# Optimization experiments

Hardware: AMD Instinct MI355X
Metric: run time of the kernel (lower is better)

## Reference

```python
import jax, jax.numpy as jnp
import numpy as np

B, SQ, SKV, D, H = 2, 2048, 2048, 1024, 16
DH = D // H


def setup_inputs() -> dict:
    key = jax.random.key(0)
    ks = jax.random.split(key, 4)
    s = 0.02
    return {
        "query_input": jax.random.normal(ks[0], (B, SQ, D), jnp.float32),
        "kv_input": jax.random.normal(ks[1], (B, SKV, D), jnp.float32),
        "Wq": jax.random.normal(ks[2], (D, D), jnp.float32) * s,
        "bq": jnp.zeros((D,), jnp.float32),
        "Wkv": jax.random.normal(ks[3], (D, 2 * D), jnp.float32) * s,
        "bkv": jnp.zeros((2 * D,), jnp.float32),
        "Wo": jax.random.normal(jax.random.fold_in(key, 7), (D, D), jnp.float32) * s,
        "bo": jnp.zeros((D,), jnp.float32),
    }


def reference(query_input, kv_input, Wq, bq, Wkv, bkv, Wo, bo):
    scale = 1.0 / jnp.sqrt(jnp.float32(DH))
    # Projections
    q = query_input @ Wq + bq                      # [B, SQ, D]
    kv = kv_input @ Wkv + bkv                      # [B, SKV, 2D]
    k, v = jnp.split(kv, 2, axis=-1)               # [B, SKV, D] each
    # Split heads: [B, H, S, DH]
    q = q.reshape(B, SQ, H, DH).transpose(0, 2, 1, 3)
    k = k.reshape(B, SKV, H, DH).transpose(0, 2, 1, 3)
    v = v.reshape(B, SKV, H, DH).transpose(0, 2, 1, 3)
    # Scores S = QK^T / sqrt(d_k)
    scores = jnp.einsum("bhqd,bhkd->bhqk", q, k) * scale
    attn = jax.nn.softmax(scores, axis=-1)
    out = jnp.einsum("bhqk,bhkd->bhqd", attn, v)   # [B, H, SQ, DH]
    out = out.transpose(0, 2, 1, 3).reshape(B, SQ, D)
    return out @ Wo + bo
```

## Files before the change

### kernel.cpp

```cpp
#include <hip/hip_runtime.h>

typedef unsigned short u16;
typedef unsigned int u32;
typedef __bf16 bf16x8 __attribute__((ext_vector_type(8)));
typedef float f32x4 __attribute__((ext_vector_type(4)));

#define QSCALE 0.18033688011112f

__device__ __forceinline__ u16 f2bf(float f) {
  u32 u = __builtin_bit_cast(u32, f);
  u += 0x7fffu + ((u >> 16) & 1u);
  return (u16)(u >> 16);
}

__device__ __forceinline__ bf16x8 as_bf16x8(uint4 v) {
  return __builtin_bit_cast(bf16x8, v);
}

__device__ __forceinline__ void async16(const void* g, void* l) {
  __builtin_amdgcn_global_load_lds(
      (__attribute__((address_space(1))) void*)(g),
      (__attribute__((address_space(3))) void*)(l), 16, 0, 0);
}

__global__ void prep_kernel(const float* __restrict__ xq, const float* __restrict__ xkv,
                            const float* __restrict__ Wq, const float* __restrict__ Wkv,
                            const float* __restrict__ Wo,
                            u16* __restrict__ Xq16, u16* __restrict__ Xkv16,
                            u16* __restrict__ WqT, u16* __restrict__ WkvT,
                            u16* __restrict__ WoT) {
  const int bid = blockIdx.x, tid = threadIdx.x;
  if (bid < 8192) {
    int i = bid * 256 + tid;
    const float* s; u16* d; int j;
    if (i < 1048576) { s = xq; d = Xq16; j = i; }
    else             { s = xkv; d = Xkv16; j = i - 1048576; }
    float4 v = ((const float4*)s)[j];
    ushort4 o;
    o.x = f2bf(v.x); o.y = f2bf(v.y); o.z = f2bf(v.z); o.w = f2bf(v.w);
    ((ushort4*)d)[j] = o;
    return;
  }
  const int b2 = bid - 8192;
  const int z = b2 >> 11, rem = b2 & 2047;
  const int by = rem >> 6, bx = rem & 63;
  const float* src; u16* dst; int Nd;
  if (z == 0)      { src = Wq;  dst = WqT;  Nd = 1024; }
  else if (z == 1) { src = Wkv; dst = WkvT; Nd = 2048; }
  else             { src = Wo;  dst = WoT;  Nd = 1024; }
  const int n0 = bx * 32, k0 = by * 32;
  if (n0 >= Nd) return;
  __shared__ float tile[32][33];
  const int tx = tid & 31, ty = tid >> 5;
#pragma unroll
  for (int j = 0; j < 4; ++j)
    tile[ty + 8 * j][tx] = src[(size_t)(k0 + ty + 8 * j) * Nd + n0 + tx];
  __syncthreads();
#pragma unroll
  for (int j = 0; j < 4; ++j)
    dst[(size_t)(n0 + ty + 8 * j) * 1024 + k0 + tx] = f2bf(tile[tx][ty + 8 * j]);
}

template <int MI>
static __device__ __forceinline__ void gemm_core(
    const u16* __restrict__ A, const u16* __restrict__ Bt, int m0,
    uint4* sA, uint4* sB, f32x4 (*acc)[4]) {
  const int tid = threadIdx.x;
  const int wv = tid >> 6, lane = tid & 63;
  const int quad = lane >> 4, l16 = lane & 15;
  const int wm = (wv >> 1) * (MI * 16), wn = (wv & 1) * 64;

  const int ib0 = wv * 128 + lane, ib1 = ib0 + 64;
  const int br0 = ib0 >> 2, bc0 = (ib0 & 3) ^ ((br0 >> 1) & 3);
  const int br1 = ib1 >> 2, bc1 = (ib1 & 3) ^ ((br1 >> 1) & 3);
  const u16* gB0 = Bt + (size_t)br0 * 1024 + bc0 * 8;
  const u16* gB1 = Bt + (size_t)br1 * 1024 + bc1 * 8;

  const int ia0 = wv * (MI * 32) + lane;
  const int ar0 = ia0 >> 2, ac0 = (ia0 & 3) ^ ((ar0 >> 1) & 3);
  const u16* gA0 = A + (size_t)(m0 + ar0) * 1024 + ac0 * 8;
  const int ia1 = ia0 + 64;
  const int ar1 = ia1 >> 2, ac1 = (ia1 & 3) ^ ((ar1 >> 1) & 3);
  const u16* gA1 = A + (size_t)(m0 + ar1) * 1024 + ac1 * 8;
  uint4* sAw = sA + wv * (MI * 32);
  uint4* sBw = sB + wv * 128;

  for (int k0 = 0; k0 < 1024; k0 += 32) {
    __syncthreads();
    async16(gA0 + k0, sAw);
    if (MI == 4) async16(gA1 + k0, sAw + 64);
    async16(gB0 + k0, sBw);
    async16(gB1 + k0, sBw + 64);
    __syncthreads();

    bf16x8 af[MI], bfr[4];
#pragma unroll
    for (int mi = 0; mi < MI; ++mi) {
      int r = wm + mi * 16 + l16;
      af[mi] = as_bf16x8(sA[r * 4 + (quad ^ ((r >> 1) & 3))]);
    }
#pragma unroll
    for (int ni = 0; ni < 4; ++ni) {
      int r = wn + ni * 16 + l16;
      bfr[ni] = as_bf16x8(sB[r * 4 + (quad ^ ((r >> 1) & 3))]);
    }
#pragma unroll
    for (int mi = 0; mi < MI; ++mi)
#pragma unroll
      for (int ni = 0; ni < 4; ++ni)
        acc[mi][ni] = __builtin_amdgcn_mfma_f32_16x16x32_bf16(
            af[mi], bfr[ni], acc[mi][ni], 0, 0, 0);
  }
}

__global__ __launch_bounds__(256, 2) void gemm_qkv(
    const u16* __restrict__ Xq, const u16* __restrict__ Xkv,
    const u16* __restrict__ WqT, const u16* __restrict__ WkvT,
    const float* __restrict__ bq, const float* __restrict__ bkv,
    u16* __restrict__ Qd, u16* __restrict__ Kd, u16* __restrict__ Vd) {
  __shared__ uint4 sA[512], sB[512];
  f32x4 acc[4][4] = {};
  const int n0 = blockIdx.x * 128, m0 = blockIdx.y * 128;
  const u16* A = (n0 < 1024) ? Xq : Xkv;
  const u16* Bt = (n0 < 1024) ? (WqT + (size_t)n0 * 1024)
                              : (WkvT + (size_t)(n0 - 1024) * 1024);
  const float* bias = (n0 < 1024) ? (bq + n0) : (bkv + (n0 - 1024));
  gemm_core<4>(A, Bt, m0, sA, sB, acc);

  const int tid = threadIdx.x, wv = tid >> 6, lane = tid & 63;
  const int quad = lane >> 4, l16 = lane & 15;
  const int wm = (wv >> 1) * 64, wn = (wv & 1) * 64;
  const int bb = m0 >> 11;
  const int gmb = m0 + wm + quad * 4;
  const int ssb = (m0 & 2047) + wm + quad * 4;
#pragma unroll
  for (int ni = 0; ni < 4; ++ni) {
    const int gn = n0 + wn + ni * 16 + l16;
    const float bvn = bias[wn + ni * 16 + l16];
    if (gn < 1024) {
      u16* base = Qd + gn;
#pragma unroll
      for (int mi = 0; mi < 4; ++mi)
#pragma unroll
        for (int r = 0; r < 4; ++r)
          base[(size_t)(gmb + mi * 16 + r) * 1024] = f2bf((acc[mi][ni][r] + bvn) * QSCALE);
    } else if (gn < 2048) {
      u16* base = Kd + (gn - 1024);
#pragma unroll
      for (int mi = 0; mi < 4; ++mi)
#pragma unroll
        for (int r = 0; r < 4; ++r)
          base[(size_t)(gmb + mi * 16 + r) * 1024] = f2bf(acc[mi][ni][r] + bvn);
    } else {
      const int col = gn - 2048, hh = col >> 6, dh = col & 63;
      u16* base = Vd + ((size_t)(bb * 16 + hh) * 64 + dh) * 2048 + ssb;
#pragma unroll
      for (int mi = 0; mi < 4; ++mi) {
        ushort4 o;
        o.x = f2bf(acc[mi][ni][0] + bvn);
        o.y = f2bf(acc[mi][ni][1] + bvn);
        o.z = f2bf(acc[mi][ni][2] + bvn);
        o.w = f2bf(acc[mi][ni][3] + bvn);
        *(ushort4*)(base + mi * 16) = o;
      }
    }
  }
}

__global__ __launch_bounds__(128, 3) void flash_attn(
    const u16* __restrict__ Q, const u16* __restrict__ K,
    const u16* __restrict__ V, u16* __restrict__ O) {
  __shared__ uint4 sK[512];
  __shared__ uint4 sV[512];
  __shared__ __align__(16) u16 sP[2][32][72];

  const int tid = threadIdx.x;
  const int wv = tid >> 6, lane = tid & 63;
  const int quad = lane >> 4, l16 = lane & 15;
  const int q0 = blockIdx.x * 64;
  const int h = blockIdx.y;

  const u16* Qb = Q + ((size_t)(blockIdx.z * 2048 + q0)) * 1024 + h * 64;
  const u16* Kb = K + ((size_t)(blockIdx.z * 2048)) * 1024 + h * 64;
  const u16* Vb = V + ((size_t)(blockIdx.z * 16 + h)) * 64 * 2048;

  bf16x8 qf[2][2];
#pragma unroll
  for (int rb = 0; rb < 2; ++rb) {
    const uint4* qp = (const uint4*)(Qb + (size_t)(wv * 32 + rb * 16 + l16) * 1024);
    qf[rb][0] = as_bf16x8(qp[quad]);
    qf[rb][1] = as_bf16x8(qp[4 + quad]);
  }

  f32x4 oacc[2][4] = {};
  f32x4 lsum[2] = {};
  const uint4 ones4 = {0x3F803F80u, 0x3F803F80u, 0x3F803F80u, 0x3F803F80u};
  const bf16x8 ones = as_bf16x8(ones4);

  const u16* gK[4]; const u16* gV[4];
#pragma unroll
  for (int j = 0; j < 4; ++j) {
    int i = wv * 256 + j * 64 + lane;
    int r = i >> 3;
    int ck = (i & 7) ^ ((r >> 2) & 7);
    int cv = (i & 7) ^ (r & 7);
    gK[j] = Kb + (size_t)r * 1024 + ck * 8;
    gV[j] = Vb + (size_t)r * 2048 + cv * 8;
  }
  uint4* sKw = sK + wv * 256;
  uint4* sVw = sV + wv * 256;

  for (int t = 0; t < 32; ++t) {
    const int skv0 = t * 64;
    __syncthreads();
#pragma unroll
    for (int j = 0; j < 4; ++j) {
      async16(gK[j] + (size_t)skv0 * 1024, sKw + j * 64);
      async16(gV[j] + skv0, sVw + j * 64);
    }
    __syncthreads();

    bf16x8 bK0[4], bK1[4];
#pragma unroll
    for (int ni = 0; ni < 4; ++ni) {
      int rr = l16 * 4 + ni;
      bK0[ni] = as_bf16x8(sK[rr * 8 + (quad ^ (l16 & 7))]);
      bK1[ni] = as_bf16x8(sK[rr * 8 + ((4 + quad) ^ (l16 & 7))]);
    }

#pragma unroll
    for (int rb = 0; rb < 2; ++rb) {
      f32x4 s4[4];
#pragma unroll
      for (int ni = 0; ni < 4; ++ni) {
        f32x4 a = {0.f, 0.f, 0.f, 0.f};
        a = __builtin_amdgcn_mfma_f32_16x16x32_bf16(qf[rb][0], bK0[ni], a, 0, 0, 0);
        a = __builtin_amdgcn_mfma_f32_16x16x32_bf16(qf[rb][1], bK1[ni], a, 0, 0, 0);
        s4[ni] = a;
      }
#pragma unroll
      for (int r = 0; r < 4; ++r) {
        u32 u0 = __builtin_bit_cast(u32, exp2f(s4[0][r])) + 0x8000u;
        u32 u1 = __builtin_bit_cast(u32, exp2f(s4[1][r])) + 0x8000u;
        u32 u2 = __builtin_bit_cast(u32, exp2f(s4[2][r])) + 0x8000u;
        u32 u3 = __builtin_bit_cast(u32, exp2f(s4[3][r])) + 0x8000u;
        uint2 pk;
        pk.x = (u0 >> 16) | (u1 & 0xFFFF0000u);
        pk.y = (u2 >> 16) | (u3 & 0xFFFF0000u);
        *(uint2*)&sP[wv][rb * 16 + quad * 4 + r][l16 * 4] = pk;
      }
    }

    bf16x8 vf0[4], vf1[4];
#pragma unroll
    for (int ni = 0; ni < 4; ++ni) {
      int rr = ni * 16 + l16;
      vf0[ni] = as_bf16x8(sV[rr * 8 + (quad ^ (rr & 7))]);
      vf1[ni] = as_bf16x8(sV[rr * 8 + ((4 + quad) ^ (rr & 7))]);
    }
#pragma unroll
    for (int rb = 0; rb < 2; ++rb) {
      bf16x8 pf0 = as_bf16x8(*(const uint4*)&sP[wv][rb * 16 + l16][quad * 8]);
      bf16x8 pf1 = as_bf16x8(*(const uint4*)&sP[wv][rb * 16 + l16][32 + quad * 8]);
      lsum[rb] = __builtin_amdgcn_mfma_f32_16x16x32_bf16(pf0, ones, lsum[rb], 0, 0, 0);
      lsum[rb] = __builtin_amdgcn_mfma_f32_16x16x32_bf16(pf1, ones, lsum[rb], 0, 0, 0);
#pragma unroll
      for (int ni = 0; ni < 4; ++ni) {
        oacc[rb][ni] = __builtin_amdgcn_mfma_f32_16x16x32_bf16(pf0, vf0[ni], oacc[rb][ni], 0, 0, 0);
        oacc[rb][ni] = __builtin_amdgcn_mfma_f32_16x16x32_bf16(pf1, vf1[ni], oacc[rb][ni], 0, 0, 0);
      }
    }
  }

#pragma unroll
  for (int rb = 0; rb < 2; ++rb) {
    u16* Ob = O + ((size_t)(blockIdx.z * 2048 + q0 + wv * 32 + rb * 16 + quad * 4)) * 1024
                + h * 64;
#pragma unroll
    for (int r = 0; r < 4; ++r) {
      float rl = 1.0f / lsum[rb][r];
#pragma unroll
      for (int ni = 0; ni < 4; ++ni)
        Ob[(size_t)r * 1024 + ni * 16 + l16] = f2bf(oacc[rb][ni][r] * rl);
    }
  }
}

__global__ __launch_bounds__(256, 2) void gemm_out(
    const u16* __restrict__ A, const u16* __restrict__ Bt,
    const float* __restrict__ bias, float* __restrict__ C) {
  __shared__ uint4 sA[256], sB[512];
  f32x4 acc[2][4] = {};
  const int n0 = blockIdx.x * 128, m0 = blockIdx.y * 64;
  gemm_core<2>(A, Bt + (size_t)n0 * 1024, m0, sA, sB, acc);

  const int tid = threadIdx.x, wv = tid >> 6, lane = tid & 63;
  const int quad = lane >> 4, l16 = lane & 15;
  const int wm = (wv >> 1) * 32, wn = (wv & 1) * 64;
  float bv[4];
#pragma unroll
  for (int ni = 0; ni < 4; ++ni) bv[ni] = bias[n0 + wn + ni * 16 + l16];
#pragma unroll
  for (int mi = 0; mi < 2; ++mi)
#pragma unroll
    for (int ni = 0; ni < 4; ++ni)
#pragma unroll
      for (int r = 0; r < 4; ++r) {
        int gm = m0 + wm + mi * 16 + quad * 4 + r;
        int gn = n0 + wn + ni * 16 + l16;
        C[(size_t)gm * 1024 + gn] = acc[mi][ni][r] + bv[ni];
      }
}

extern "C" void kernel_launch(void* const* d_in, const int* in_sizes, int n_in,
                              void* d_out, int out_size, void* d_ws, size_t ws_size,
                              hipStream_t stream) {
  const float* xq  = (const float*)d_in[0];
  const float* xkv = (const float*)d_in[1];
  const float* Wq  = (const float*)d_in[2];
  const float* bq  = (const float*)d_in[3];
  const float* Wkv = (const float*)d_in[4];
  const float* bkv = (const float*)d_in[5];
  const float* Wo  = (const float*)d_in[6];
  const float* bo  = (const float*)d_in[7];
  float* out = (float*)d_out;

  char* p = (char*)d_ws;
  u16* Xq16  = (u16*)p; p += (size_t)8 << 20;
  u16* Xkv16 = (u16*)p; p += (size_t)8 << 20;
  u16* WqT   = (u16*)p; p += (size_t)2 << 20;
  u16* WkvT  = (u16*)p; p += (size_t)4 << 20;
  u16* WoT   = (u16*)p; p += (size_t)2 << 20;
  u16* Q16   = (u16*)p; p += (size_t)8 << 20;
  u16* K16   = (u16*)p; p += (size_t)8 << 20;
  u16* Vt16  = (u16*)p; p += (size_t)8 << 20;
  u16* O16   = (u16*)p; p += (size_t)8 << 20;

  prep_kernel<<<14336, 256, 0, stream>>>(xq, xkv, Wq, Wkv, Wo,
                                         Xq16, Xkv16, WqT, WkvT, WoT);
  gemm_qkv<<<dim3(24, 32), 256, 0, stream>>>(Xq16, Xkv16, WqT, WkvT, bq, bkv,
                                             Q16, K16, Vt16);
  flash_attn<<<dim3(32, 16, 2), 128, 0, stream>>>(Q16, K16, Vt16, O16);
  gemm_out<<<dim3(8, 64), 256, 0, stream>>>(O16, WoT, bo, out);
}
```

Baseline: 235.0 us.

## Load K/V straight into registers and software-pipeline attention without block barriers

The flash attention kernel no longer stages K and V tiles through shared memory with async loads and two __syncthreads per tile. Each wave now loads its MFMA operand fragments directly from global memory into registers. The loop is software-pipelined: the next K tile is loaded while the previous tile's P·V runs, and the P tile is double-buffered in shared memory. This removes barrier stalls and the LDS round trip. In exchange, the two waves of a block each fetch the full K/V tiles, which doubles global/L2 traffic, the global access pattern is strided, and the launch bound drops from 3 to 2 blocks per unit.

```diff
diff --git a/kernel.cpp b/kernel.cpp
--- a/kernel.cpp
+++ b/kernel.cpp
@@ -167,27 +167,25 @@
   }
 }
 
-__global__ __launch_bounds__(128, 3) void flash_attn(
+__global__ __launch_bounds__(128, 2) void flash_attn(
     const u16* __restrict__ Q, const u16* __restrict__ K,
     const u16* __restrict__ V, u16* __restrict__ O) {
-  __shared__ uint4 sK[512];
-  __shared__ uint4 sV[512];
-  __shared__ __align__(16) u16 sP[2][32][72];
+  __shared__ __align__(16) u16 sP[2][64][72];
 
   const int tid = threadIdx.x;
   const int wv = tid >> 6, lane = tid & 63;
   const int quad = lane >> 4, l16 = lane & 15;
-  const int q0 = blockIdx.x * 64;
-  const int h = blockIdx.y;
-
-  const u16* Qb = Q + ((size_t)(blockIdx.z * 2048 + q0)) * 1024 + h * 64;
-  const u16* Kb = K + ((size_t)(blockIdx.z * 2048)) * 1024 + h * 64;
-  const u16* Vb = V + ((size_t)(blockIdx.z * 16 + h)) * 64 * 2048;
+  const int q0 = blockIdx.x * 64 + wv * 32;
+  const int h = blockIdx.y, b = blockIdx.z;
+
+  const u16* Qb = Q + ((size_t)(b * 2048 + q0)) * 1024 + h * 64;
+  const u16* Kb = K + ((size_t)b * 2048 + 4 * l16) * 1024 + h * 64 + quad * 8;
+  const u16* Vb = V + ((size_t)(b * 16 + h) * 64 + l16) * 2048 + quad * 8;
 
   bf16x8 qf[2][2];
 #pragma unroll
   for (int rb = 0; rb < 2; ++rb) {
-    const uint4* qp = (const uint4*)(Qb + (size_t)(wv * 32 + rb * 16 + l16) * 1024);
+    const uint4* qp = (const uint4*)(Qb + (size_t)(rb * 16 + l16) * 1024);
     qf[rb][0] = as_bf16x8(qp[quad]);
     qf[rb][1] = as_bf16x8(qp[4 + quad]);
   }
@@ -197,45 +195,33 @@
   const uint4 ones4 = {0x3F803F80u, 0x3F803F80u, 0x3F803F80u, 0x3F803F80u};
   const bf16x8 ones = as_bf16x8(ones4);
 
-  const u16* gK[4]; const u16* gV[4];
-#pragma unroll
-  for (int j = 0; j < 4; ++j) {
-    int i = wv * 256 + j * 64 + lane;
-    int r = i >> 3;
-    int ck = (i & 7) ^ ((r >> 2) & 7);
-    int cv = (i & 7) ^ (r & 7);
-    gK[j] = Kb + (size_t)r * 1024 + ck * 8;
-    gV[j] = Vb + (size_t)r * 2048 + cv * 8;
-  }
-  uint4* sKw = sK + wv * 256;
-  uint4* sVw = sV + wv * 256;
-
-  for (int t = 0; t < 32; ++t) {
-    const int skv0 = t * 64;
-    __syncthreads();
-#pragma unroll
-    for (int j = 0; j < 4; ++j) {
-      async16(gK[j] + (size_t)skv0 * 1024, sKw + j * 64);
-      async16(gV[j] + skv0, sVw + j * 64);
-    }
-    __syncthreads();
-
-    bf16x8 bK0[4], bK1[4];
+  bf16x8 kreg[2][4], vreg[2][4];
+
+  auto loadK = [&](int t) {
+    const u16* kp = Kb + (size_t)t * 65536;
 #pragma unroll
     for (int ni = 0; ni < 4; ++ni) {
-      int rr = l16 * 4 + ni;
-      bK0[ni] = as_bf16x8(sK[rr * 8 + (quad ^ (l16 & 7))]);
-      bK1[ni] = as_bf16x8(sK[rr * 8 + ((4 + quad) ^ (l16 & 7))]);
-    }
-
+      kreg[0][ni] = as_bf16x8(*(const uint4*)(kp + ni * 1024));
+      kreg[1][ni] = as_bf16x8(*(const uint4*)(kp + ni * 1024 + 32));
+    }
+  };
+  auto loadV = [&](int t) {
+    const u16* vp = Vb + t * 64;
+#pragma unroll
+    for (int ni = 0; ni < 4; ++ni) {
+      vreg[0][ni] = as_bf16x8(*(const uint4*)(vp + ni * 32768));
+      vreg[1][ni] = as_bf16x8(*(const uint4*)(vp + ni * 32768 + 32));
+    }
+  };
+  auto qk_exp = [&](int buf) {
 #pragma unroll
     for (int rb = 0; rb < 2; ++rb) {
       f32x4 s4[4];
 #pragma unroll
       for (int ni = 0; ni < 4; ++ni) {
         f32x4 a = {0.f, 0.f, 0.f, 0.f};
-        a = __builtin_amdgcn_mfma_f32_16x16x32_bf16(qf[rb][0], bK0[ni], a, 0, 0, 0);
-        a = __builtin_amdgcn_mfma_f32_16x16x32_bf16(qf[rb][1], bK1[ni], a, 0, 0, 0);
+        a = __builtin_amdgcn_mfma_f32_16x16x32_bf16(qf[rb][0], kreg[0][ni], a, 0, 0, 0);
+        a = __builtin_amdgcn_mfma_f32_16x16x32_bf16(qf[rb][1], kreg[1][ni], a, 0, 0, 0);
         s4[ni] = a;
       }
 #pragma unroll
@@ -247,35 +233,39 @@
         uint2 pk;
         pk.x = (u0 >> 16) | (u1 & 0xFFFF0000u);
         pk.y = (u2 >> 16) | (u3 & 0xFFFF0000u);
-        *(uint2*)&sP[wv][rb * 16 + quad * 4 + r][l16 * 4] = pk;
-      }
-    }
-
-    bf16x8 vf0[4], vf1[4];
-#pragma unroll
-    for (int ni = 0; ni < 4; ++ni) {
-      int rr = ni * 16 + l16;
-      vf0[ni] = as_bf16x8(sV[rr * 8 + (quad ^ (rr & 7))]);
-      vf1[ni] = as_bf16x8(sV[rr * 8 + ((4 + quad) ^ (rr & 7))]);
-    }
+        *(uint2*)&sP[buf][wv * 32 + rb * 16 + quad * 4 + r][l16 * 4] = pk;
+      }
+    }
+  };
+  auto pv = [&](int buf) {
 #pragma unroll
     for (int rb = 0; rb < 2; ++rb) {
-      bf16x8 pf0 = as_bf16x8(*(const uint4*)&sP[wv][rb * 16 + l16][quad * 8]);
-      bf16x8 pf1 = as_bf16x8(*(const uint4*)&sP[wv][rb * 16 + l16][32 + quad * 8]);
+      bf16x8 pf0 = as_bf16x8(*(const uint4*)&sP[buf][wv * 32 + rb * 16 + l16][quad * 8]);
+      bf16x8 pf1 = as_bf16x8(*(const uint4*)&sP[buf][wv * 32 + rb * 16 + l16][32 + quad * 8]);
       lsum[rb] = __builtin_amdgcn_mfma_f32_16x16x32_bf16(pf0, ones, lsum[rb], 0, 0, 0);
       lsum[rb] = __builtin_amdgcn_mfma_f32_16x16x32_bf16(pf1, ones, lsum[rb], 0, 0, 0);
 #pragma unroll
       for (int ni = 0; ni < 4; ++ni) {
-        oacc[rb][ni] = __builtin_amdgcn_mfma_f32_16x16x32_bf16(pf0, vf0[ni], oacc[rb][ni], 0, 0, 0);
-        oacc[rb][ni] = __builtin_amdgcn_mfma_f32_16x16x32_bf16(pf1, vf1[ni], oacc[rb][ni], 0, 0, 0);
-      }
-    }
-  }
+        oacc[rb][ni] = __builtin_amdgcn_mfma_f32_16x16x32_bf16(pf0, vreg[0][ni], oacc[rb][ni], 0, 0, 0);
+        oacc[rb][ni] = __builtin_amdgcn_mfma_f32_16x16x32_bf16(pf1, vreg[1][ni], oacc[rb][ni], 0, 0, 0);
+      }
+    }
+  };
+
+  loadK(0);
+  loadV(0);
+  qk_exp(0);
+  for (int t = 1; t < 32; ++t) {
+    loadK(t);
+    pv((t - 1) & 1);
+    loadV(t);
+    qk_exp(t & 1);
+  }
+  pv(1);
 
 #pragma unroll
   for (int rb = 0; rb < 2; ++rb) {
-    u16* Ob = O + ((size_t)(blockIdx.z * 2048 + q0 + wv * 32 + rb * 16 + quad * 4)) * 1024
-                + h * 64;
+    u16* Ob = O + ((size_t)(b * 2048 + q0 + rb * 16 + quad * 4)) * 1024 + h * 64;
 #pragma unroll
     for (int r = 0; r < 4; ++r) {
       float rl = 1.0f / lsum[rb][r];
```

Result: slower. 284.9 us (+21.2%).
